# Performance work log

Measured on AMD Instinct MI355X. Metric: run time of the kernel, lower is better.

Reference implementation:

```python
import jax, jax.numpy as jnp
import numpy as np

T, B, A = 32, 16, 8
XA, XL, XS = 16, 32, 4
LF, LK = 9, 3                     # lidar conv out channels / kernel
EF = 64                           # entity_features == attention embed dim
HEADS, HD = 4, 16
LI, LH = 128, 128                 # lstm input / hidden
NK = [16, 16, 16]                 # entities per type
DK = [16, 24, 32]                 # raw feature dim per type
ZL = LF * (XL - LK + 1)           # 270: Conv1d has padding=0 (padding_mode inert)
S = XA + ZL + XS                  # 290: width of x_self


def setup_inputs():
    key = jax.random.key(0)
    ks = iter(jax.random.split(key, 64))
    n = lambda shape, s=1.0: jax.random.normal(next(ks), shape, jnp.float32) * s
    inp = {
        "x_agent": n((T, B, A, XA)),
        "x_lidar": n((T, B, A, XL)),
        "x_safe_zone": n((T, B, A, XS)),
    }
    for i, (nk, dk) in enumerate(zip(NK, DK)):
        inp[f"ent_feats_{i}"] = n((T, B, A, nk, dk))
        inp[f"ent_mask_{i}"] = jax.random.bernoulli(next(ks), 0.7, (T, B, A, nk)).astype(jnp.float32)
    inp["done"] = jax.random.bernoulli(next(ks), 0.05, (T, B)).astype(jnp.float32)
    inp["h0"] = jnp.zeros((B, A, LH), jnp.float32)
    inp["c0"] = jnp.zeros((B, A, LH), jnp.float32)
    w = lambda *shape: n(shape, 0.05)
    zb = lambda m: jnp.zeros((m,), jnp.float32)
    inp.update(
        lidar_w=w(LF, 1, LK), lidar_b=zb(LF),
        self_w=w(EF, 2 * S), self_b=zb(EF),
        ent_w0=w(EF, DK[0] + S), ent_b0=zb(EF),
        ent_w1=w(EF, DK[1] + S), ent_b1=zb(EF),
        ent_w2=w(EF, DK[2] + S), ent_b2=zb(EF),
        in_proj_w=w(3 * EF, EF), in_proj_b=zb(3 * EF),
        out_proj_w=w(EF, EF), out_proj_b=zb(EF),
        sa_w=w(EF, EF), sa_b=zb(EF),
        pool_w=w(LI, S + EF), pool_b=zb(LI),
        w_ih=w(4 * LH, LI), w_hh=w(4 * LH, LH),
        b_ih=zb(4 * LH), b_hh=zb(4 * LH),
        head_w=w(1, LH), head_b=zb(1),
    )
    return inp


def reference(x_agent, x_lidar, x_safe_zone,
              ent_feats_0, ent_feats_1, ent_feats_2,
              ent_mask_0, ent_mask_1, ent_mask_2,
              done, h0, c0,
              lidar_w, lidar_b, self_w, self_b,
              ent_w0, ent_b0, ent_w1, ent_b1, ent_w2, ent_b2,
              in_proj_w, in_proj_b, out_proj_w, out_proj_b,
              sa_w, sa_b, pool_w, pool_b,
              w_ih, w_hh, b_ih, b_hh, head_w, head_b):
    Tn, Bn, An = x_agent.shape[:3]
    M = Tn * Bn * An
    # lidar Conv1d, VALID (torch default padding=0)
    xl = x_lidar.reshape(M, 1, XL)
    zl = jax.nn.relu(jax.lax.conv_general_dilated(
        xl, lidar_w, (1,), [(0, 0)], dimension_numbers=('NCH', 'OIH', 'NCH'))
        + lidar_b[None, :, None])                       # (M, LF, XL-LK+1)
    zl = zl.reshape(Tn, Bn, An, ZL)
    x_self = jnp.concatenate([x_agent, zl, x_safe_zone], -1)   # (T,B,A,S)
    z_self = jax.nn.relu(jnp.concatenate([x_self, x_self], -1) @ self_w.T + self_b)
    z_list = [z_self[..., None, :]]                           # (T,B,A,1,EF)
    m_list = [jnp.ones(x_self.shape[:3] + (1,), x_self.dtype)]
    for feats, mask, wk, bk in ((ent_feats_0, ent_mask_0, ent_w0, ent_b0),
                                (ent_feats_1, ent_mask_1, ent_w1, ent_b1),
                                (ent_feats_2, ent_mask_2, ent_w2, ent_b2)):
        xs = jnp.broadcast_to(x_self[..., None, :], feats.shape[:4] + (x_self.shape[-1],))
        z_list.append(jax.nn.relu(jnp.concatenate([feats, xs], -1) @ wk.T + bk))
        m_list.append(mask)
    z_ent = jnp.concatenate(z_list, -2)                        # (T,B,A,E,EF)
    mvec = jnp.concatenate(m_list, -1)                         # (T,B,A,E)
    E = z_ent.shape[-2]
    # multihead self-attention with key_padding_mask = (mask == 0)
    zf = z_ent.reshape(M, E, EF)
    q, k, v = jnp.split(zf @ in_proj_w.T + in_proj_b, 3, axis=-1)
    sh = lambda t: t.reshape(M, E, HEADS, HD).transpose(0, 2, 1, 3)   # (M,H,E,hd)
    q, k, v = sh(q), sh(k), sh(v)
    scores = jnp.einsum('mhqd,mhkd->mhqk', q, k) / np.float32(np.sqrt(HD))
    pad = (mvec.reshape(M, E) == 0.0)[:, None, None, :]
    attn = jax.nn.softmax(jnp.where(pad, jnp.float32(-1e9), scores), axis=-1)
    sa = jnp.einsum('mhqk,mhkd->mhqd', attn, v).transpose(0, 2, 1, 3).reshape(M, E, EF)
    sa = (sa @ out_proj_w.T + out_proj_b).reshape(Tn, Bn, An, E, EF)
    res = z_ent + jax.nn.relu(sa @ sa_w.T + sa_b)
    z_pool = jnp.mean(res * mvec[..., None], axis=-2)          # (T,B,A,EF), mean over E
    z = jax.nn.relu(jnp.concatenate([x_self, z_pool], -1) @ pool_w.T + pool_b)  # (T,B,A,LI)
    # per-timestep LSTM with done-reset fused into a single scan
    def step(carry, xt):
        h, c = carry
        x_t, d_t = xt                     # (B,A,LI), (B,)
        keep = (1.0 - d_t)[:, None, None]
        h, c = h * keep, c * keep
        g = x_t @ w_ih.T + h @ w_hh.T + (b_ih + b_hh)
        i, f, gg, o = jnp.split(g, 4, -1)  # torch gate order i,f,g,o
        c = jax.nn.sigmoid(f) * c + jax.nn.sigmoid(i) * jnp.tanh(gg)
        h = jax.nn.sigmoid(o) * jnp.tanh(c)
        return (h, c), h
    _, hs = jax.lax.scan(step, (h0, c0), (z, done))            # hs: (T,B,A,LH)
    value = hs @ head_w.T + head_b                             # (T,B,A,1)
    return value[..., 0]
```

## Files before the change

### kernel.cpp

```cpp
#include <hip/hip_runtime.h>
#include <math.h>

constexpr size_t XCH_OFF  = 0;
constexpr size_t XCL_OFF  = 786432;
constexpr size_t P_OFF    = 1572864;
constexpr size_t GX_OFF   = 0;
constexpr size_t WPH_OFF  = 2621440;
constexpr size_t WPL_OFF  = 2662400;
constexpr size_t BP_OFF   = 2703360;
constexpr size_t WF_OFF   = 2703616;
constexpr size_t QKV_OFF  = 2708224;
constexpr size_t WO_OFF   = 2714368;
constexpr size_t WSA_OFF  = 2716416;
constexpr size_t PWH_OFF  = 2718464;
constexpr size_t PWL_OFF  = 2743040;
constexpr size_t ZH_OFF   = 2767616;
constexpr size_t ZL_OFF   = 3029760;
constexpr size_t WIHH_OFF = 3291904;
constexpr size_t WIHL_OFF = 3324672;
constexpr size_t BG_OFF   = 3357440;

typedef float f32x4 __attribute__((ext_vector_type(4)));
typedef __bf16 bf16x8v __attribute__((ext_vector_type(8)));
typedef unsigned short us8 __attribute__((ext_vector_type(8)));
union b8u { us8 u; bf16x8v b; };

static __device__ __forceinline__ float sigf(float x) { return 1.0f / (1.0f + __expf(-x)); }

static __device__ __forceinline__ unsigned short f2b(float x) {
  unsigned int u = __float_as_uint(x);
  unsigned int r = (u + 0x7FFFu + ((u >> 16) & 1u)) >> 16;
  return (unsigned short)r;
}
static __device__ __forceinline__ float b2f(unsigned short s) {
  return __uint_as_float(((unsigned int)s) << 16);
}
static __device__ __forceinline__ bf16x8v ld_bf8(const unsigned short* p) {
  b8u c; c.u = *(const us8*)p; return c.b;
}

__global__ __launch_bounds__(256) void k_prep(
    const float* __restrict__ self_w, const float* __restrict__ self_b,
    const float* __restrict__ e0w, const float* __restrict__ e0b,
    const float* __restrict__ e1w, const float* __restrict__ e1b,
    const float* __restrict__ e2w, const float* __restrict__ e2b,
    const float* __restrict__ ipw, const float* __restrict__ opw,
    const float* __restrict__ saw, const float* __restrict__ plw,
    const float* __restrict__ wih, const float* __restrict__ bih,
    const float* __restrict__ bhh, float* __restrict__ ws)
{
  unsigned short* WPH  = (unsigned short*)(ws + WPH_OFF);
  unsigned short* WPL  = (unsigned short*)(ws + WPL_OFF);
  unsigned short* QKVF = (unsigned short*)(ws + QKV_OFF);
  unsigned short* WOF  = (unsigned short*)(ws + WO_OFF);
  unsigned short* WSAF = (unsigned short*)(ws + WSA_OFF);
  unsigned short* PWH  = (unsigned short*)(ws + PWH_OFF);
  unsigned short* PWL  = (unsigned short*)(ws + PWL_OFF);
  unsigned short* WIHH = (unsigned short*)(ws + WIHH_OFF);
  unsigned short* WIHL = (unsigned short*)(ws + WIHL_OFF);
  const int N_WP = 16 * 10 * 512, N_PW = 8 * 12 * 512, N_WIH = 32 * 4 * 512;
  const int total = N_WP + 256 + 4608 + 12288 + 4096 + 4096 + N_PW + N_WIH + 512;
  for (int idx = blockIdx.x * 256 + threadIdx.x; idx < total; idx += gridDim.x * 256) {
    int i = idx;
    if (i < N_WP) {
      int ct = i / (10 * 512), rem = i % (10 * 512);
      int ktg = rem >> 9, e = rem & 511, ll = e >> 3, j = e & 7;
      int k = ktg * 32 + 8 * (ll >> 4) + j;
      int n = ct * 16 + (ll & 15);
      float v = 0.f;
      if (k < 290) {
        if (n < 64)       v = self_w[n * 580 + k] + self_w[n * 580 + 290 + k];
        else if (n < 128) v = e0w[(n - 64) * 306 + 16 + k];
        else if (n < 192) v = e1w[(n - 128) * 314 + 24 + k];
        else              v = e2w[(n - 192) * 322 + 32 + k];
      }
      unsigned short h = f2b(v);
      WPH[i] = h; WPL[i] = f2b(v - b2f(h)); continue;
    }
    i -= N_WP;
    if (i < 256) {
      float v;
      if (i < 64) v = self_b[i];
      else if (i < 128) v = e0b[i - 64];
      else if (i < 192) v = e1b[i - 128];
      else v = e2b[i - 192];
      ws[BP_OFF + i] = v; continue;
    }
    i -= 256;
    if (i < 4608) {
      float v;
      if (i < 1024)      { int d = i >> 6, n = i & 63; v = e0w[n * 306 + d]; }
      else if (i < 2560) { int q = i - 1024, d = q >> 6, n = q & 63; v = e1w[n * 314 + d]; }
      else               { int q = i - 2560, d = q >> 6, n = q & 63; v = e2w[n * 322 + d]; }
      ws[WF_OFF + i] = v; continue;
    }
    i -= 4608;
    if (i < 12288) {
      int ct = i >> 10, kt = (i >> 9) & 1, ll = (i >> 3) & 63, j = i & 7;
      int d = kt * 32 + 8 * (ll >> 4) + j;
      int n = ct * 16 + (ll & 15);
      QKVF[i] = f2b(ipw[n * 64 + d]); continue;
    }
    i -= 12288;
    if (i < 4096) {
      int ct = i >> 10, kt = (i >> 9) & 1, ll = (i >> 3) & 63, j = i & 7;
      int d = kt * 32 + 8 * (ll >> 4) + j;
      int n = ct * 16 + (ll & 15);
      WOF[i] = f2b(opw[n * 64 + d]); continue;
    }
    i -= 4096;
    if (i < 4096) {
      int ct = i >> 10, kt = (i >> 9) & 1, ll = (i >> 3) & 63, j = i & 7;
      int d = kt * 32 + 8 * (ll >> 4) + j;
      int n = ct * 16 + (ll & 15);
      WSAF[i] = f2b(saw[n * 64 + d]); continue;
    }
    i -= 4096;
    if (i < N_PW) {
      int ct = i / (12 * 512), rem = i % (12 * 512);
      int ktg = rem >> 9, e = rem & 511, ll = e >> 3, j = e & 7;
      int k = ktg * 32 + 8 * (ll >> 4) + j;
      int n = ct * 16 + (ll & 15);
      float v = (k < 354) ? plw[n * 354 + k] : 0.f;
      unsigned short h = f2b(v);
      PWH[i] = h; PWL[i] = f2b(v - b2f(h)); continue;
    }
    i -= N_PW;
    if (i < N_WIH) {
      int ct = i / (4 * 512), rem = i % (4 * 512);
      int ktg = rem >> 9, e = rem & 511, ll = e >> 3, j = e & 7;
      int k = ktg * 32 + 8 * (ll >> 4) + j;
      int n = ct * 16 + (ll & 15);
      float v = wih[n * 128 + k];
      unsigned short h = f2b(v);
      WIHH[i] = h; WIHL[i] = f2b(v - b2f(h)); continue;
    }
    i -= N_WIH;
    ws[BG_OFF + i] = bih[i] + bhh[i];
  }
}

__global__ __launch_bounds__(256) void k_assemble(
    const float* __restrict__ xa, const float* __restrict__ xl, const float* __restrict__ xs,
    const float* __restrict__ lw, const float* __restrict__ lb,
    unsigned short* __restrict__ xch, unsigned short* __restrict__ xcl)
{
  const int total = 4096 * 320;
  for (int idx = blockIdx.x * 256 + threadIdx.x; idx < total; idx += gridDim.x * 256) {
    int m = idx / 320, j = idx - m * 320;
    if (j >= 290) {
      int c = 354 + (j - 290);
      xch[(size_t)m * 384 + c] = 0; xcl[(size_t)m * 384 + c] = 0; continue;
    }
    float v;
    if (j < 16) v = xa[m * 16 + j];
    else if (j < 286) {
      int jj = j - 16; int c = jj / 30; int p = jj - c * 30;
      const float* xr = xl + m * 32 + p;
      v = lw[c * 3] * xr[0] + lw[c * 3 + 1] * xr[1] + lw[c * 3 + 2] * xr[2] + lb[c];
      v = fmaxf(v, 0.f);
    } else v = xs[m * 4 + (j - 286)];
    unsigned short h = f2b(v);
    xch[(size_t)m * 384 + j] = h;
    xcl[(size_t)m * 384 + j] = f2b(v - b2f(h));
  }
}

__global__ __launch_bounds__(256) void k_bgemm(
    const unsigned short* __restrict__ Ah, const unsigned short* __restrict__ Al, int ldaK,
    const unsigned short* __restrict__ Bh, const unsigned short* __restrict__ Bl,
    const float* __restrict__ bias, int Kpad, int N, int reluN,
    float* __restrict__ Cf, unsigned short* __restrict__ Chi, unsigned short* __restrict__ Clo,
    int mode)
{
  __shared__ unsigned short AhS[64 * 72], AlS[64 * 72];
  int m0 = blockIdx.x * 64;
  int tid = threadIdx.x, w = tid >> 6, l = tid & 63, lr = l & 15, lg = l >> 4;
  int ctg = blockIdx.y * 4 + w;
  int nKt = Kpad >> 5;
  f32x4 acc[4] = {};
  int srow = tid >> 2, sseg = tid & 3;
  for (int k0 = 0; k0 < Kpad; k0 += 64) {
    {
      const us8* gh = (const us8*)&Ah[(size_t)(m0 + srow) * ldaK + k0 + sseg * 16];
      const us8* gl_ = (const us8*)&Al[(size_t)(m0 + srow) * ldaK + k0 + sseg * 16];
      us8 h0 = gh[0], h1 = gh[1], l0 = gl_[0], l1 = gl_[1];
      *(us8*)&AhS[srow * 72 + sseg * 16]     = h0;
      *(us8*)&AhS[srow * 72 + sseg * 16 + 8] = h1;
      *(us8*)&AlS[srow * 72 + sseg * 16]     = l0;
      *(us8*)&AlS[srow * 72 + sseg * 16 + 8] = l1;
    }
    __syncthreads();
    #pragma unroll
    for (int kt = 0; kt < 2; ++kt) {
      int ktg = (k0 >> 5) + kt;
      bf16x8v bh = ld_bf8(&Bh[((size_t)(ctg * nKt + ktg) * 64 + l) * 8]);
      bf16x8v bl = ld_bf8(&Bl[((size_t)(ctg * nKt + ktg) * 64 + l) * 8]);
      #pragma unroll
      for (int rt = 0; rt < 4; ++rt) {
        bf16x8v ah = ld_bf8(&AhS[(rt * 16 + lr) * 72 + kt * 32 + 8 * lg]);
        bf16x8v al = ld_bf8(&AlS[(rt * 16 + lr) * 72 + kt * 32 + 8 * lg]);
        acc[rt] = __builtin_amdgcn_mfma_f32_16x16x32_bf16(ah, bh, acc[rt], 0, 0, 0);
        acc[rt] = __builtin_amdgcn_mfma_f32_16x16x32_bf16(al, bh, acc[rt], 0, 0, 0);
        acc[rt] = __builtin_amdgcn_mfma_f32_16x16x32_bf16(ah, bl, acc[rt], 0, 0, 0);
      }
    }
    __syncthreads();
  }
  int n = ctg * 16 + lr;
  float bs = bias[n];
  #pragma unroll
  for (int rt = 0; rt < 4; ++rt) {
    #pragma unroll
    for (int i = 0; i < 4; ++i) {
      int row = m0 + rt * 16 + lg * 4 + i;
      float v = acc[rt][i] + bs;
      if (n < reluN) v = fmaxf(v, 0.f);
      if (mode == 0) Cf[(size_t)row * N + n] = v;
      else {
        unsigned short h = f2b(v);
        Chi[(size_t)row * N + n] = h;
        Clo[(size_t)row * N + n] = f2b(v - b2f(h));
      }
    }
  }
}

template <int DK>
static __device__ __forceinline__ void ent_encode(
    const float* __restrict__ fP, const float* __restrict__ WF,
    const float* __restrict__ xsP, unsigned short* __restrict__ zh, int m, int w, int l, int t)
{
  float wreg[DK];
  #pragma unroll
  for (int d = 0; d < DK; ++d) wreg[d] = WF[d * 64 + l];
  float xb = xsP[64 + t * 64 + l];
  #pragma unroll
  for (int i = 0; i < 4; ++i) {
    int er = w + 4 * i;
    const float* fr = fP + (size_t)(m * 16 + er) * DK;
    float acc = xb;
    #pragma unroll
    for (int d4 = 0; d4 < DK / 4; ++d4) {
      float4 f4 = reinterpret_cast<const float4*>(fr)[d4];
      acc += f4.x * wreg[4 * d4] + f4.y * wreg[4 * d4 + 1] + f4.z * wreg[4 * d4 + 2] + f4.w * wreg[4 * d4 + 3];
    }
    zh[(1 + t * 16 + er) * 72 + l] = f2b(fmaxf(acc, 0.f));
  }
}

__global__ __launch_bounds__(256, 3) void k_attn(
    const float* __restrict__ Pmat,
    const float* __restrict__ f0, const float* __restrict__ f1, const float* __restrict__ f2,
    const float* __restrict__ mk0, const float* __restrict__ mk1, const float* __restrict__ mk2,
    const float* __restrict__ WF,
    const unsigned short* __restrict__ QKVF,
    const unsigned short* __restrict__ WOF,
    const unsigned short* __restrict__ WSAF,
    const float* __restrict__ ipb, const float* __restrict__ opb, const float* __restrict__ sab_,
    unsigned short* __restrict__ xch, unsigned short* __restrict__ xcl)
{
  __shared__ unsigned short smem[26856];
  unsigned short* zh  = smem;
  unsigned short* qh  = smem + 3528;
  unsigned short* kh  = smem + 8136;
  float*          xsP = (float*)(smem + 12744);
  unsigned short* pl  = smem + 3528;
  unsigned short* vt  = smem + 17640;
  unsigned short* sah = smem + 22248;
  unsigned short* oh  = kh;
  int m = blockIdx.x;
  int tid = threadIdx.x, w = tid >> 6, l = tid & 63;
  int lr = l & 15, lg = l >> 4;
  b8u zz;
  #pragma unroll
  for (int i = 0; i < 8; ++i) zz.u[i] = 0;
  bf16x8v zero8 = zz.b;

  float mvr[16];
  {
    float pv = Pmat[(size_t)m * 256 + tid];
    xsP[tid] = pv;
    if (tid < 64) zh[tid] = f2b(pv);
    #pragma unroll
    for (int rt = 0; rt < 4; ++rt)
      #pragma unroll
      for (int ii = 0; ii < 4; ++ii) {
        int key = rt * 16 + 4 * lg + ii;
        float v;
        if (key == 0) v = 1.f;
        else if (key < 17) v = mk0[m * 16 + key - 1];
        else if (key < 33) v = mk1[m * 16 + key - 17];
        else if (key < 49) v = mk2[m * 16 + key - 33];
        else v = 0.f;
        mvr[rt * 4 + ii] = v;
      }
  }
  __syncthreads();

  ent_encode<16>(f0, WF + 0,    xsP, zh, m, w, l, 0);
  ent_encode<24>(f1, WF + 1024, xsP, zh, m, w, l, 1);
  ent_encode<32>(f2, WF + 2560, xsP, zh, m, w, l, 2);
  __syncthreads();

  {
    bf16x8v za[4][2];
    #pragma unroll
    for (int rt = 0; rt < 4; ++rt)
      #pragma unroll
      for (int kt = 0; kt < 2; ++kt) {
        bf16x8v t = ld_bf8(&zh[(rt * 16 + lr) * 72 + kt * 32 + 8 * lg]);
        za[rt][kt] = (rt * 16 + lr < 49) ? t : zero8;
      }
    #pragma unroll
    for (int cc = 0; cc < 3; ++cc) {
      int ct = w + 4 * cc;
      bf16x8v b0 = ld_bf8(&QKVF[((ct * 2 + 0) * 64 + l) * 8]);
      bf16x8v b1 = ld_bf8(&QKVF[((ct * 2 + 1) * 64 + l) * 8]);
      int n = ct * 16 + lr;
      float bias = ipb[n];
      #pragma unroll
      for (int rt = 0; rt < 4; ++rt) {
        f32x4 acc = {0.f, 0.f, 0.f, 0.f};
        acc = __builtin_amdgcn_mfma_f32_16x16x32_bf16(za[rt][0], b0, acc, 0, 0, 0);
        acc = __builtin_amdgcn_mfma_f32_16x16x32_bf16(za[rt][1], b1, acc, 0, 0, 0);
        #pragma unroll
        for (int i = 0; i < 4; ++i) {
          int r = rt * 16 + lg * 4 + i;
          float val = acc[i] + bias;
          if (cc == 0)      qh[r * 72 + n] = f2b(val);
          else if (cc == 1) kh[r * 72 + (n - 64)] = f2b(val);
          else { int hd = n - 128; vt[(hd >> 4) * 1152 + (hd & 15) * 72 + r] = f2b(val); }
        }
      }
    }
  }
  __syncthreads();

  float pst[4][16];
  {
    int h = w;
    bf16x8v ka[4], qb[4];
    #pragma unroll
    for (int rt = 0; rt < 4; ++rt) {
      bf16x8v t = ld_bf8(&kh[(rt * 16 + lr) * 72 + h * 16 + 8 * (lg & 1)]);
      ka[rt] = (lg < 2) ? t : zero8;
    }
    #pragma unroll
    for (int ct = 0; ct < 4; ++ct) {
      bf16x8v t = ld_bf8(&qh[(ct * 16 + lr) * 72 + h * 16 + 8 * (lg & 1)]);
      qb[ct] = (lg < 2) ? t : zero8;
    }
    #pragma unroll
    for (int ct = 0; ct < 4; ++ct)
      #pragma unroll
      for (int rt = 0; rt < 4; ++rt) {
        f32x4 acc = {0.f, 0.f, 0.f, 0.f};
        acc = __builtin_amdgcn_mfma_f32_16x16x32_bf16(ka[rt], qb[ct], acc, 0, 0, 0);
        #pragma unroll
        for (int i = 0; i < 4; ++i) pst[ct][rt * 4 + i] = acc[i];
      }
    #pragma unroll
    for (int ct = 0; ct < 4; ++ct) {
      float mx = -1e30f;
      #pragma unroll
      for (int k16 = 0; k16 < 16; ++k16) {
        float x = pst[ct][k16] * 0.25f;
        pst[ct][k16] = x;
        if (mvr[k16] != 0.f) mx = fmaxf(mx, x);
      }
      mx = fmaxf(mx, __shfl_xor(mx, 16, 64));
      mx = fmaxf(mx, __shfl_xor(mx, 32, 64));
      float sum = 0.f;
      #pragma unroll
      for (int k16 = 0; k16 < 16; ++k16) {
        float p = (mvr[k16] != 0.f) ? __expf(pst[ct][k16] - mx) : 0.f;
        pst[ct][k16] = p;
        sum += p;
      }
      sum += __shfl_xor(sum, 16, 64);
      sum += __shfl_xor(sum, 32, 64);
      float inv = 1.f / sum;
      #pragma unroll
      for (int k16 = 0; k16 < 16; ++k16) pst[ct][k16] *= inv;
    }
  }
  __syncthreads();
  {
    int h = w;
    unsigned short* ph = pl + h * 3528;
    #pragma unroll
    for (int ct = 0; ct < 4; ++ct) {
      int q = ct * 16 + lr;
      if (q < 49) {
        #pragma unroll
        for (int rt = 0; rt < 4; ++rt)
          #pragma unroll
          for (int ii = 0; ii < 4; ++ii)
            ph[q * 72 + rt * 16 + 4 * lg + ii] = f2b(pst[ct][rt * 4 + ii]);
      }
    }
  }
  __syncthreads();
  {
    int h = w;
    const unsigned short* ph = pl + h * 3528;
    bf16x8v va0 = ld_bf8(&vt[h * 1152 + lr * 72 + 8 * lg]);
    bf16x8v va1 = ld_bf8(&vt[h * 1152 + lr * 72 + 32 + 8 * lg]);
    #pragma unroll
    for (int ct = 0; ct < 4; ++ct) {
      bf16x8v pb0 = ld_bf8(&ph[(ct * 16 + lr) * 72 + 8 * lg]);
      bf16x8v pb1 = ld_bf8(&ph[(ct * 16 + lr) * 72 + 32 + 8 * lg]);
      f32x4 o = {0.f, 0.f, 0.f, 0.f};
      o = __builtin_amdgcn_mfma_f32_16x16x32_bf16(va0, pb0, o, 0, 0, 0);
      o = __builtin_amdgcn_mfma_f32_16x16x32_bf16(va1, pb1, o, 0, 0, 0);
      int q = ct * 16 + lr;
      #pragma unroll
      for (int i = 0; i < 4; ++i)
        sah[q * 72 + h * 16 + 4 * lg + i] = f2b(o[i]);
    }
  }
  __syncthreads();

  {
    int ct = w, n = ct * 16 + lr;
    bf16x8v b0 = ld_bf8(&WOF[((ct * 2 + 0) * 64 + l) * 8]);
    bf16x8v b1 = ld_bf8(&WOF[((ct * 2 + 1) * 64 + l) * 8]);
    float bias = opb[n];
    #pragma unroll
    for (int rt = 0; rt < 4; ++rt) {
      bf16x8v a0 = ld_bf8(&sah[(rt * 16 + lr) * 72 + 8 * lg]);
      bf16x8v a1 = ld_bf8(&sah[(rt * 16 + lr) * 72 + 32 + 8 * lg]);
      f32x4 acc = {0.f, 0.f, 0.f, 0.f};
      acc = __builtin_amdgcn_mfma_f32_16x16x32_bf16(a0, b0, acc, 0, 0, 0);
      acc = __builtin_amdgcn_mfma_f32_16x16x32_bf16(a1, b1, acc, 0, 0, 0);
      #pragma unroll
      for (int i = 0; i < 4; ++i) {
        int r = rt * 16 + lg * 4 + i;
        if (r < 49) oh[r * 72 + n] = f2b(acc[i] + bias);
      }
    }
  }
  __syncthreads();

  {
    int ct = w, n = ct * 16 + lr;
    bf16x8v b0 = ld_bf8(&WSAF[((ct * 2 + 0) * 64 + l) * 8]);
    bf16x8v b1 = ld_bf8(&WSAF[((ct * 2 + 1) * 64 + l) * 8]);
    float bias = sab_[n];
    float pacc = 0.f;
    #pragma unroll
    for (int rt = 0; rt < 4; ++rt) {
      bf16x8v a0 = ld_bf8(&oh[(rt * 16 + lr) * 72 + 8 * lg]);
      bf16x8v a1 = ld_bf8(&oh[(rt * 16 + lr) * 72 + 32 + 8 * lg]);
      f32x4 acc = {0.f, 0.f, 0.f, 0.f};
      acc = __builtin_amdgcn_mfma_f32_16x16x32_bf16(a0, b0, acc, 0, 0, 0);
      acc = __builtin_amdgcn_mfma_f32_16x16x32_bf16(a1, b1, acc, 0, 0, 0);
      #pragma unroll
      for (int i = 0; i < 4; ++i) {
        int r = rt * 16 + lg * 4 + i;
        if (r < 49) {
          float val = fmaxf(acc[i] + bias, 0.f);
          float z = b2f(zh[r * 72 + n]);
          pacc += (z + val) * mvr[rt * 4 + i];
        }
      }
    }
    pacc += __shfl_xor(pacc, 16, 64);
    pacc += __shfl_xor(pacc, 32, 64);
    if (lg == 0) {
      float y = pacc * (1.0f / 49.0f);
      unsigned short h = f2b(y);
      xch[(size_t)m * 384 + 290 + n] = h;
      xcl[(size_t)m * 384 + 290 + n] = f2b(y - b2f(h));
    }
  }
}

__global__ __launch_bounds__(512) void k_lstm(
    const float* __restrict__ Gx, const float* __restrict__ whh,
    const float* __restrict__ done, const float* __restrict__ h0, const float* __restrict__ c0,
    const float* __restrict__ hw, const float* __restrict__ hb, float* __restrict__ out)
{
  __shared__ float h[128], c[128], gl[512], red[2];
  int s = blockIdx.x, b = s >> 3;
  int g = threadIdx.x;
  float wreg[128];
  {
    const float4* w4 = reinterpret_cast<const float4*>(whh + (size_t)g * 128);
    #pragma unroll
    for (int j4 = 0; j4 < 32; ++j4) {
      float4 f4 = w4[j4];
      wreg[4 * j4] = f4.x; wreg[4 * j4 + 1] = f4.y; wreg[4 * j4 + 2] = f4.z; wreg[4 * j4 + 3] = f4.w;
    }
  }
  if (g < 128) { h[g] = h0[s * 128 + g]; c[g] = c0[s * 128 + g]; }
  __syncthreads();
  for (int t = 0; t < 32; ++t) {
    float keep = 1.f - done[t * 16 + b];
    float acc = 0.f;
    const float4* h4 = reinterpret_cast<const float4*>(h);
    #pragma unroll
    for (int j4 = 0; j4 < 32; ++j4) {
      float4 f4 = h4[j4];
      acc += f4.x * wreg[4 * j4] + f4.y * wreg[4 * j4 + 1] + f4.z * wreg[4 * j4 + 2] + f4.w * wreg[4 * j4 + 3];
    }
    gl[g] = Gx[(size_t)(t * 128 + s) * 512 + g] + keep * acc;
    __syncthreads();
    if (g < 128) {
      float iv = sigf(gl[g]);
      float fv = sigf(gl[128 + g]);
      float gg = tanhf(gl[256 + g]);
      float ov = sigf(gl[384 + g]);
      float cn = fv * (c[g] * keep) + iv * gg;
      float hn = ov * tanhf(cn);
      c[g] = cn; h[g] = hn;
      float pv = hn * hw[g];
      #pragma unroll
      for (int off = 32; off > 0; off >>= 1) pv += __shfl_down(pv, off, 64);
      if ((g & 63) == 0) red[g >> 6] = pv;
    }
    __syncthreads();
    if (g == 0) out[t * 128 + s] = red[0] + red[1] + hb[0];
  }
}

extern "C" void kernel_launch(void* const* d_in, const int* in_sizes, int n_in,
                              void* d_out, int out_size, void* d_ws, size_t ws_size,
                              hipStream_t stream) {
  const float* x_agent = (const float*)d_in[0];
  const float* x_lidar = (const float*)d_in[1];
  const float* x_safe  = (const float*)d_in[2];
  const float* ef0 = (const float*)d_in[3];
  const float* em0 = (const float*)d_in[4];
  const float* ef1 = (const float*)d_in[5];
  const float* em1 = (const float*)d_in[6];
  const float* ef2 = (const float*)d_in[7];
  const float* em2 = (const float*)d_in[8];
  const float* done = (const float*)d_in[9];
  const float* h0 = (const float*)d_in[10];
  const float* c0 = (const float*)d_in[11];
  const float* lw = (const float*)d_in[12];
  const float* lb = (const float*)d_in[13];
  const float* self_w = (const float*)d_in[14];
  const float* self_b = (const float*)d_in[15];
  const float* e0w = (const float*)d_in[16];
  const float* e0b = (const float*)d_in[17];
  const float* e1w = (const float*)d_in[18];
  const float* e1b = (const float*)d_in[19];
  const float* e2w = (const float*)d_in[20];
  const float* e2b = (const float*)d_in[21];
  const float* ipw = (const float*)d_in[22];
  const float* ipb = (const float*)d_in[23];
  const float* opw = (const float*)d_in[24];
  const float* opb = (const float*)d_in[25];
  const float* saw = (const float*)d_in[26];
  const float* sab = (const float*)d_in[27];
  const float* plw = (const float*)d_in[28];
  const float* plb = (const float*)d_in[29];
  const float* wih = (const float*)d_in[30];
  const float* whh = (const float*)d_in[31];
  const float* bih = (const float*)d_in[32];
  const float* bhh = (const float*)d_in[33];
  const float* hw  = (const float*)d_in[34];
  const float* hb  = (const float*)d_in[35];
  float* ws  = (float*)d_ws;
  float* out = (float*)d_out;

  unsigned short* XCH = (unsigned short*)(ws + XCH_OFF);
  unsigned short* XCL = (unsigned short*)(ws + XCL_OFF);

  k_prep<<<256, 256, 0, stream>>>(self_w, self_b, e0w, e0b, e1w, e1b, e2w, e2b,
                                  ipw, opw, saw, plw, wih, bih, bhh, ws);
  k_assemble<<<2048, 256, 0, stream>>>(x_agent, x_lidar, x_safe, lw, lb, XCH, XCL);
  {
    dim3 g(64, 4);
    k_bgemm<<<g, 256, 0, stream>>>(XCH, XCL, 384,
                                   (const unsigned short*)(ws + WPH_OFF),
                                   (const unsigned short*)(ws + WPL_OFF),
                                   ws + BP_OFF, 320, 256, 64,
                                   ws + P_OFF, nullptr, nullptr, 0);
  }
  k_attn<<<4096, 256, 0, stream>>>(ws + P_OFF, ef0, ef1, ef2, em0, em1, em2,
                                   ws + WF_OFF,
                                   (const unsigned short*)(ws + QKV_OFF),
                                   (const unsigned short*)(ws + WO_OFF),
                                   (const unsigned short*)(ws + WSA_OFF),
                                   ipb, opb, sab, XCH, XCL);
  {
    dim3 g(64, 2);
    k_bgemm<<<g, 256, 0, stream>>>(XCH, XCL, 384,
                                   (const unsigned short*)(ws + PWH_OFF),
                                   (const unsigned short*)(ws + PWL_OFF),
                                   plb, 384, 128, 128,
                                   nullptr,
                                   (unsigned short*)(ws + ZH_OFF),
                                   (unsigned short*)(ws + ZL_OFF), 1);
  }
  {
    dim3 g(64, 8);
    k_bgemm<<<g, 256, 0, stream>>>((const unsigned short*)(ws + ZH_OFF),
                                   (const unsigned short*)(ws + ZL_OFF), 128,
                                   (const unsigned short*)(ws + WIHH_OFF),
                                   (const unsigned short*)(ws + WIHL_OFF),
                                   ws + BG_OFF, 128, 512, 0,
                                   ws + GX_OFF, nullptr, nullptr, 0);
  }
  k_lstm<<<128, 512, 0, stream>>>(ws + GX_OFF, whh, done, h0, c0, hw, hb, out);
}
```

Measured before the change: 293.6 us.

## Use bf16 MFMA for entity encoding, fold score scale into K, prefetch Gx

Entity feature encoding in the attention kernel moves from per-lane fp32 FMA loops to a single bf16 MFMA per entity type. The weights are prepacked as bf16 fragments in the prep kernel. The 0.25 attention scale is folded into the K projection, which removes a multiply pass over the scores. The LSTM kernel also prefetches the next timestep's Gx row into a register to hide its global-load latency. The cost is reduced precision: entity features and weights are rounded to bf16 where they were fp32 before.

After: 280.5 us. 4.4% less time.

```diff
diff --git a/kernel.cpp b/kernel.cpp
--- a/kernel.cpp
+++ b/kernel.cpp
@@ -51,6 +51,7 @@
 {
   unsigned short* WPH  = (unsigned short*)(ws + WPH_OFF);
   unsigned short* WPL  = (unsigned short*)(ws + WPL_OFF);
+  unsigned short* WFF  = (unsigned short*)(ws + WF_OFF);
   unsigned short* QKVF = (unsigned short*)(ws + QKV_OFF);
   unsigned short* WOF  = (unsigned short*)(ws + WO_OFF);
   unsigned short* WSAF = (unsigned short*)(ws + WSA_OFF);
@@ -59,7 +60,7 @@
   unsigned short* WIHH = (unsigned short*)(ws + WIHH_OFF);
   unsigned short* WIHL = (unsigned short*)(ws + WIHL_OFF);
   const int N_WP = 16 * 10 * 512, N_PW = 8 * 12 * 512, N_WIH = 32 * 4 * 512;
-  const int total = N_WP + 256 + 4608 + 12288 + 4096 + 4096 + N_PW + N_WIH + 512;
+  const int total = N_WP + 256 + 6144 + 12288 + 4096 + 4096 + N_PW + N_WIH + 512;
   for (int idx = blockIdx.x * 256 + threadIdx.x; idx < total; idx += gridDim.x * 256) {
     int i = idx;
     if (i < N_WP) {
@@ -87,14 +88,18 @@
       ws[BP_OFF + i] = v; continue;
     }
     i -= 256;
-    if (i < 4608) {
-      float v;
-      if (i < 1024)      { int d = i >> 6, n = i & 63; v = e0w[n * 306 + d]; }
-      else if (i < 2560) { int q = i - 1024, d = q >> 6, n = q & 63; v = e1w[n * 314 + d]; }
-      else               { int q = i - 2560, d = q >> 6, n = q & 63; v = e2w[n * 322 + d]; }
-      ws[WF_OFF + i] = v; continue;
-    }
-    i -= 4608;
+    if (i < 6144) {
+      int t2 = i >> 11, rem = i & 2047;
+      int ct = rem >> 9, e = rem & 511, ll = e >> 3, j = e & 7;
+      int k = 8 * (ll >> 4) + j;
+      int n = ct * 16 + (ll & 15);
+      float v = 0.f;
+      if (t2 == 0)      { if (k < 16) v = e0w[n * 306 + k]; }
+      else if (t2 == 1) { if (k < 24) v = e1w[n * 314 + k]; }
+      else              { if (k < 32) v = e2w[n * 322 + k]; }
+      WFF[i] = f2b(v); continue;
+    }
+    i -= 6144;
     if (i < 12288) {
       int ct = i >> 10, kt = (i >> 9) & 1, ll = (i >> 3) & 63, j = i & 7;
       int d = kt * 32 + 8 * (ll >> 4) + j;
@@ -226,34 +231,11 @@
   }
 }
 
-template <int DK>
-static __device__ __forceinline__ void ent_encode(
-    const float* __restrict__ fP, const float* __restrict__ WF,
-    const float* __restrict__ xsP, unsigned short* __restrict__ zh, int m, int w, int l, int t)
-{
-  float wreg[DK];
-  #pragma unroll
-  for (int d = 0; d < DK; ++d) wreg[d] = WF[d * 64 + l];
-  float xb = xsP[64 + t * 64 + l];
-  #pragma unroll
-  for (int i = 0; i < 4; ++i) {
-    int er = w + 4 * i;
-    const float* fr = fP + (size_t)(m * 16 + er) * DK;
-    float acc = xb;
-    #pragma unroll
-    for (int d4 = 0; d4 < DK / 4; ++d4) {
-      float4 f4 = reinterpret_cast<const float4*>(fr)[d4];
-      acc += f4.x * wreg[4 * d4] + f4.y * wreg[4 * d4 + 1] + f4.z * wreg[4 * d4 + 2] + f4.w * wreg[4 * d4 + 3];
-    }
-    zh[(1 + t * 16 + er) * 72 + l] = f2b(fmaxf(acc, 0.f));
-  }
-}
-
 __global__ __launch_bounds__(256, 3) void k_attn(
     const float* __restrict__ Pmat,
     const float* __restrict__ f0, const float* __restrict__ f1, const float* __restrict__ f2,
     const float* __restrict__ mk0, const float* __restrict__ mk1, const float* __restrict__ mk2,
-    const float* __restrict__ WF,
+    const unsigned short* __restrict__ WFF,
     const unsigned short* __restrict__ QKVF,
     const unsigned short* __restrict__ WOF,
     const unsigned short* __restrict__ WSAF,
@@ -298,9 +280,33 @@
   }
   __syncthreads();
 
-  ent_encode<16>(f0, WF + 0,    xsP, zh, m, w, l, 0);
-  ent_encode<24>(f1, WF + 1024, xsP, zh, m, w, l, 1);
-  ent_encode<32>(f2, WF + 2560, xsP, zh, m, w, l, 2);
+  {
+    const float* fps[3] = {f0, f1, f2};
+    #pragma unroll
+    for (int t = 0; t < 3; ++t) {
+      const int DK = (t == 0) ? 16 : (t == 1) ? 24 : 32;
+      bf16x8v a;
+      if (8 * lg < DK) {
+        const float4* fr4 = reinterpret_cast<const float4*>(
+            fps[t] + ((size_t)m * 16 + lr) * DK + 8 * lg);
+        float4 fa = fr4[0], fb = fr4[1];
+        b8u c;
+        c.u[0] = f2b(fa.x); c.u[1] = f2b(fa.y); c.u[2] = f2b(fa.z); c.u[3] = f2b(fa.w);
+        c.u[4] = f2b(fb.x); c.u[5] = f2b(fb.y); c.u[6] = f2b(fb.z); c.u[7] = f2b(fb.w);
+        a = c.b;
+      } else a = zero8;
+      bf16x8v b = ld_bf8(&WFF[(t * 4 + w) * 512 + l * 8]);
+      f32x4 acc = {0.f, 0.f, 0.f, 0.f};
+      acc = __builtin_amdgcn_mfma_f32_16x16x32_bf16(a, b, acc, 0, 0, 0);
+      int n = w * 16 + lr;
+      float xb = xsP[64 + t * 64 + n];
+      #pragma unroll
+      for (int i = 0; i < 4; ++i) {
+        int er = 4 * lg + i;
+        zh[(1 + t * 16 + er) * 72 + n] = f2b(fmaxf(acc[i] + xb, 0.f));
+      }
+    }
+  }
   __syncthreads();
 
   {
@@ -329,7 +335,7 @@
           int r = rt * 16 + lg * 4 + i;
           float val = acc[i] + bias;
           if (cc == 0)      qh[r * 72 + n] = f2b(val);
-          else if (cc == 1) kh[r * 72 + (n - 64)] = f2b(val);
+          else if (cc == 1) kh[r * 72 + (n - 64)] = f2b(val * 0.25f);
           else { int hd = n - 128; vt[(hd >> 4) * 1152 + (hd & 15) * 72 + r] = f2b(val); }
         }
       }
@@ -364,11 +370,8 @@
     for (int ct = 0; ct < 4; ++ct) {
       float mx = -1e30f;
       #pragma unroll
-      for (int k16 = 0; k16 < 16; ++k16) {
-        float x = pst[ct][k16] * 0.25f;
-        pst[ct][k16] = x;
-        if (mvr[k16] != 0.f) mx = fmaxf(mx, x);
-      }
+      for (int k16 = 0; k16 < 16; ++k16)
+        if (mvr[k16] != 0.f) mx = fmaxf(mx, pst[ct][k16]);
       mx = fmaxf(mx, __shfl_xor(mx, 16, 64));
       mx = fmaxf(mx, __shfl_xor(mx, 32, 64));
       float sum = 0.f;
@@ -495,8 +498,10 @@
     }
   }
   if (g < 128) { h[g] = h0[s * 128 + g]; c[g] = c0[s * 128 + g]; }
+  float gx = Gx[(size_t)s * 512 + g];
   __syncthreads();
   for (int t = 0; t < 32; ++t) {
+    float gx_nxt = (t < 31) ? Gx[(size_t)((t + 1) * 128 + s) * 512 + g] : 0.f;
     float keep = 1.f - done[t * 16 + b];
     float acc = 0.f;
     const float4* h4 = reinterpret_cast<const float4*>(h);
@@ -505,7 +510,7 @@
       float4 f4 = h4[j4];
       acc += f4.x * wreg[4 * j4] + f4.y * wreg[4 * j4 + 1] + f4.z * wreg[4 * j4 + 2] + f4.w * wreg[4 * j4 + 3];
     }
-    gl[g] = Gx[(size_t)(t * 128 + s) * 512 + g] + keep * acc;
+    gl[g] = gx + keep * acc;
     __syncthreads();
     if (g < 128) {
       float iv = sigf(gl[g]);
@@ -522,6 +527,7 @@
     }
     __syncthreads();
     if (g == 0) out[t * 128 + s] = red[0] + red[1] + hb[0];
+    gx = gx_nxt;
   }
 }
 
@@ -582,7 +588,7 @@
                                    ws + P_OFF, nullptr, nullptr, 0);
   }
   k_attn<<<4096, 256, 0, stream>>>(ws + P_OFF, ef0, ef1, ef2, em0, em1, em2,
-                                   ws + WF_OFF,
+                                   (const unsigned short*)(ws + WF_OFF),
                                    (const unsigned short*)(ws + QKV_OFF),
                                    (const unsigned short*)(ws + WO_OFF),
                                    (const unsigned short*)(ws + WSA_OFF),
```
